# Kernel optimization log

Measured on AMD Instinct MI355X. Metric: run time of the kernel, lower is better.

## Reference

```python
import jax, jax.numpy as jnp
import numpy as np

NUM_ZONES = 256  # number of distinct zone ids per image (fill_max of zones)


def setup_inputs() -> dict:
    key = jax.random.key(0)
    k1, k2 = jax.random.split(key)
    B, H, W = 64, 512, 512
    inp = jax.random.normal(k1, (B, 1, H, W), dtype=jnp.float32)
    zones = jax.random.randint(k2, (B, H, W), 0, NUM_ZONES, dtype=jnp.int32)
    return {"input": inp, "zones": zones}


def reference(input, zones):
    # zones branch of CenterExtractor.forward: per-batch scatter_max over zone ids.
    # For each batch element, keep the pixel holding the maximum heatmap value
    # within each zone (segmented argmax), producing a boolean center mask.
    B = input.shape[0]
    x = input.reshape(B, -1)   # [B, N] flattened heatmap
    z = zones.reshape(B, -1)   # [B, N] segment ids

    # per-batch segmented max: [B, NUM_ZONES]
    seg_max = jax.vmap(
        lambda xv, zv: jax.ops.segment_max(xv, zv, num_segments=NUM_ZONES)
    )(x, z)

    # pixel is a center iff it attains its zone's max (ties measure-zero for randn;
    # empty zones have seg_max = -inf and match nothing, mirroring idxs != N filter)
    mask = x == jnp.take_along_axis(seg_max, z, axis=1)  # [B, N] bool

    centermask = mask.reshape(input.shape)  # [B, 1, H, W] bool
    n_centers = jnp.sum(centermask)
    return centermask, n_centers
```

## Files before the change

### kernel.cpp

```cpp
#include <hip/hip_runtime.h>

#define NZ    256
#define NB    64
#define NPIX  (512 * 512)

#define EPT1  32
#define CHUNK1 (256 * EPT1)
#define BPB1  (NPIX / CHUNK1)
#define NBLK1 (NB * BPB1)

#define NZP   264

#define CHUNK3 (256 * 16)
#define BPB3  (NPIX / CHUNK3)
#define NBLK3 (NB * BPB3)

__device__ __forceinline__ unsigned umax2(unsigned a, unsigned b) { return a > b ? a : b; }

__device__ __forceinline__ unsigned enc(float f) {
    unsigned b = __float_as_uint(f);
    return b ^ ((b & 0x80000000u) ? 0xFFFFFFFFu : 0x80000000u);
}
__device__ __forceinline__ float dec(unsigned u) {
    unsigned b = (u & 0x80000000u) ? (u ^ 0x80000000u) : ~u;
    return __uint_as_float(b);
}

__global__ __launch_bounds__(256) void segmax_part(
        const float* __restrict__ inp, const int* __restrict__ zones,
        unsigned* __restrict__ part) {
    __shared__ unsigned sm[4 * NZP];
    const int t = threadIdx.x;
    const int wave = t >> 6;
    for (int i = t; i < 4 * NZP; i += 256) sm[i] = 0u;
    __syncthreads();

    unsigned* mytab = &sm[wave * NZP];

    const int batch = blockIdx.x / BPB1;
    const int chunk = blockIdx.x % BPB1;
    const long base = (long)batch * NPIX + (long)chunk * CHUNK1;
    const float4* in4 = (const float4*)(inp + base);
    const int4*   z4  = (const int4*)(zones + base);

#pragma unroll
    for (int h = 0; h < EPT1 / 4; ++h) {
        float4 v = in4[h * 256 + t];
        int4   z = z4[h * 256 + t];
        atomicMax(&mytab[z.x], enc(v.x));
        atomicMax(&mytab[z.y], enc(v.y));
        atomicMax(&mytab[z.z], enc(v.z));
        atomicMax(&mytab[z.w], enc(v.w));
    }
    __syncthreads();

    unsigned m = umax2(umax2(sm[t], sm[NZP + t]),
                       umax2(sm[2 * NZP + t], sm[3 * NZP + t]));
    part[(long)blockIdx.x * NZ + t] = m;
}

__global__ __launch_bounds__(256) void segmax_reduce(
        const unsigned* __restrict__ part, float* __restrict__ segf) {
    const int t = threadIdx.x;
    const int batch = blockIdx.x;
    const unsigned* p = part + (long)batch * BPB1 * NZ;
    unsigned m = 0u;
#pragma unroll 8
    for (int c = 0; c < BPB1; ++c) m = umax2(m, p[c * NZ + t]);
    segf[batch * NZ + t] = dec(m);
}

__global__ __launch_bounds__(256) void mask_kernel(
        const float* __restrict__ inp, const int* __restrict__ zones,
        const float* __restrict__ segf,
        int* __restrict__ mask, int* __restrict__ partial) {
    __shared__ float smax[NZ];
    __shared__ int wsum[4];
    const int t = threadIdx.x;

    const int batch = blockIdx.x / BPB3;
    const int chunk = blockIdx.x % BPB3;

    smax[t] = segf[batch * NZ + t];
    __syncthreads();

    const long base = (long)batch * NPIX + (long)chunk * CHUNK3;
    const float4* in4 = (const float4*)(inp + base);
    const int4*   z4  = (const int4*)(zones + base);
    int4* m4 = (int4*)(mask + base);

    int c = 0;
#pragma unroll
    for (int it = 0; it < 4; ++it) {
        float4 v = in4[it * 256 + t];
        int4   z = z4[it * 256 + t];
        int4 m;
        m.x = (v.x == smax[z.x]) ? 1 : 0;
        m.y = (v.y == smax[z.y]) ? 1 : 0;
        m.z = (v.z == smax[z.z]) ? 1 : 0;
        m.w = (v.w == smax[z.w]) ? 1 : 0;
        m4[it * 256 + t] = m;
        c += m.x + m.y + m.z + m.w;
    }

#pragma unroll
    for (int off = 32; off; off >>= 1) c += __shfl_down(c, off);
    if ((t & 63) == 0) wsum[t >> 6] = c;
    __syncthreads();
    if (t == 0) partial[blockIdx.x] = wsum[0] + wsum[1] + wsum[2] + wsum[3];
}

__global__ __launch_bounds__(256) void count_kernel(
        const int* __restrict__ partial, int n, int* __restrict__ count) {
    __shared__ int wsum[4];
    const int t = threadIdx.x;
    int c = 0;
    for (int i = t; i < n; i += 256) c += partial[i];
#pragma unroll
    for (int off = 32; off; off >>= 1) c += __shfl_down(c, off);
    if ((t & 63) == 0) wsum[t >> 6] = c;
    __syncthreads();
    if (t == 0) *count = wsum[0] + wsum[1] + wsum[2] + wsum[3];
}

extern "C" void kernel_launch(void* const* d_in, const int* in_sizes, int n_in,
                              void* d_out, int out_size, void* d_ws, size_t ws_size,
                              hipStream_t stream) {
    const float* inp   = (const float*)d_in[0];
    const int*   zones = (const int*)d_in[1];
    int*         out   = (int*)d_out;

    unsigned* part    = (unsigned*)d_ws;
    float*    segf    = (float*)((char*)d_ws + (size_t)NBLK1 * NZ * 4);
    int*      partial = (int*)((char*)d_ws + (size_t)NBLK1 * NZ * 4 + (size_t)NB * NZ * 4);

    const long nmask = (long)NB * NPIX;

    segmax_part  <<<NBLK1, 256, 0, stream>>>(inp, zones, part);
    segmax_reduce<<<NB,    256, 0, stream>>>(part, segf);
    mask_kernel  <<<NBLK3, 256, 0, stream>>>(inp, zones, segf, out, partial);
    count_kernel <<<1,     256, 0, stream>>>(partial, NBLK3, out + nmask);
}
```

Baseline: 56.59 us.

## Replace per-block partial tables with hinted global atomicMax and drop reduce kernel

The per-wave shared atomic tables and the separate reduce kernel are removed. Each block keeps a racy shared-memory hint of the running max per zone and only issues a global atomicMax into a per-batch table when a value beats the hint. A memset clears the table first. This cuts one kernel launch, the partial-table traffic and most shared atomics. In exchange it adds global atomic contention on a small table, and the racy hint can let extra atomics through, though the result stays correct.

Measured after the change: 157.4 us. +178.1%, slower.

```diff
diff --git a/kernel.cpp b/kernel.cpp
--- a/kernel.cpp
+++ b/kernel.cpp
@@ -9,13 +9,9 @@
 #define BPB1  (NPIX / CHUNK1)
 #define NBLK1 (NB * BPB1)
 
-#define NZP   264
-
 #define CHUNK3 (256 * 16)
 #define BPB3  (NPIX / CHUNK3)
 #define NBLK3 (NB * BPB3)
-
-__device__ __forceinline__ unsigned umax2(unsigned a, unsigned b) { return a > b ? a : b; }
 
 __device__ __forceinline__ unsigned enc(float f) {
     unsigned b = __float_as_uint(f);
@@ -28,51 +24,35 @@
 
 __global__ __launch_bounds__(256) void segmax_part(
         const float* __restrict__ inp, const int* __restrict__ zones,
-        unsigned* __restrict__ part) {
-    __shared__ unsigned sm[4 * NZP];
+        unsigned* __restrict__ gtab) {
+    __shared__ unsigned hint[NZ];
     const int t = threadIdx.x;
-    const int wave = t >> 6;
-    for (int i = t; i < 4 * NZP; i += 256) sm[i] = 0u;
+    hint[t] = 0u;
     __syncthreads();
-
-    unsigned* mytab = &sm[wave * NZP];
 
     const int batch = blockIdx.x / BPB1;
     const int chunk = blockIdx.x % BPB1;
     const long base = (long)batch * NPIX + (long)chunk * CHUNK1;
     const float4* in4 = (const float4*)(inp + base);
     const int4*   z4  = (const int4*)(zones + base);
+    unsigned* __restrict__ grow = gtab + batch * NZ;
 
 #pragma unroll
     for (int h = 0; h < EPT1 / 4; ++h) {
         float4 v = in4[h * 256 + t];
         int4   z = z4[h * 256 + t];
-        atomicMax(&mytab[z.x], enc(v.x));
-        atomicMax(&mytab[z.y], enc(v.y));
-        atomicMax(&mytab[z.z], enc(v.z));
-        atomicMax(&mytab[z.w], enc(v.w));
+        unsigned e0 = enc(v.x), e1 = enc(v.y), e2 = enc(v.z), e3 = enc(v.w);
+        unsigned c0 = hint[z.x], c1 = hint[z.y], c2 = hint[z.z], c3 = hint[z.w];
+        if (e0 > c0) { hint[z.x] = e0; atomicMax(&grow[z.x], e0); }
+        if (e1 > c1) { hint[z.y] = e1; atomicMax(&grow[z.y], e1); }
+        if (e2 > c2) { hint[z.z] = e2; atomicMax(&grow[z.z], e2); }
+        if (e3 > c3) { hint[z.w] = e3; atomicMax(&grow[z.w], e3); }
     }
-    __syncthreads();
-
-    unsigned m = umax2(umax2(sm[t], sm[NZP + t]),
-                       umax2(sm[2 * NZP + t], sm[3 * NZP + t]));
-    part[(long)blockIdx.x * NZ + t] = m;
-}
-
-__global__ __launch_bounds__(256) void segmax_reduce(
-        const unsigned* __restrict__ part, float* __restrict__ segf) {
-    const int t = threadIdx.x;
-    const int batch = blockIdx.x;
-    const unsigned* p = part + (long)batch * BPB1 * NZ;
-    unsigned m = 0u;
-#pragma unroll 8
-    for (int c = 0; c < BPB1; ++c) m = umax2(m, p[c * NZ + t]);
-    segf[batch * NZ + t] = dec(m);
 }
 
 __global__ __launch_bounds__(256) void mask_kernel(
         const float* __restrict__ inp, const int* __restrict__ zones,
-        const float* __restrict__ segf,
+        const unsigned* __restrict__ gtab,
         int* __restrict__ mask, int* __restrict__ partial) {
     __shared__ float smax[NZ];
     __shared__ int wsum[4];
@@ -81,7 +61,7 @@
     const int batch = blockIdx.x / BPB3;
     const int chunk = blockIdx.x % BPB3;
 
-    smax[t] = segf[batch * NZ + t];
+    smax[t] = dec(gtab[batch * NZ + t]);
     __syncthreads();
 
     const long base = (long)batch * NPIX + (long)chunk * CHUNK3;
@@ -130,14 +110,13 @@
     const int*   zones = (const int*)d_in[1];
     int*         out   = (int*)d_out;
 
-    unsigned* part    = (unsigned*)d_ws;
-    float*    segf    = (float*)((char*)d_ws + (size_t)NBLK1 * NZ * 4);
-    int*      partial = (int*)((char*)d_ws + (size_t)NBLK1 * NZ * 4 + (size_t)NB * NZ * 4);
+    unsigned* gtab    = (unsigned*)d_ws;
+    int*      partial = (int*)((char*)d_ws + (size_t)NB * NZ * 4);
 
     const long nmask = (long)NB * NPIX;
 
-    segmax_part  <<<NBLK1, 256, 0, stream>>>(inp, zones, part);
-    segmax_reduce<<<NB,    256, 0, stream>>>(part, segf);
-    mask_kernel  <<<NBLK3, 256, 0, stream>>>(inp, zones, segf, out, partial);
-    count_kernel <<<1,     256, 0, stream>>>(partial, NBLK3, out + nmask);
+    hipMemsetAsync(gtab, 0, (size_t)NB * NZ * 4, stream);
+    segmax_part <<<NBLK1, 256, 0, stream>>>(inp, zones, gtab);
+    mask_kernel <<<NBLK3, 256, 0, stream>>>(inp, zones, gtab, out, partial);
+    count_kernel<<<1,     256, 0, stream>>>(partial, NBLK3, out + nmask);
 }
```
